# Optimization experiments

Measured on AMD Instinct MI355X. Metric: run time of the kernel, lower is better.

The kernel has to match this reference:

```python
import jax, jax.numpy as jnp
import numpy as np

C = 64  # in_dim

def _dwpw(x, w_dw, w_pw):
    # depthwise 1x1x1 conv (groups=C, no bias) == per-channel scale
    x = x * w_dw[None, :, None, None, None]
    # pointwise 1x1x1 conv (no bias) == channel mixing matmul
    return jnp.einsum('bcdhw,oc->bodhw', x, w_pw)

def setup_inputs() -> dict:
    key = jax.random.key(0)
    ks = jax.random.split(key, 8)
    B, D, H, W = 2, 16, 16, 16
    x = jax.random.normal(ks[0], (B, C, D, H, W), dtype=jnp.float32)
    s = 1.0 / np.sqrt(C)
    q_dw = jax.random.normal(ks[1], (C,), dtype=jnp.float32) * s
    q_pw = jax.random.normal(ks[2], (C, C), dtype=jnp.float32) * s
    k_dw = jax.random.normal(ks[3], (C,), dtype=jnp.float32) * s
    k_pw = jax.random.normal(ks[4], (C, C), dtype=jnp.float32) * s
    v_dw = jax.random.normal(ks[5], (C,), dtype=jnp.float32) * s
    v_pw = jax.random.normal(ks[6], (C, C), dtype=jnp.float32) * s
    gamma = jnp.zeros((1,), dtype=jnp.float32) + 0.1  # nonzero so output depends on attention
    return {"x": x, "q_dw": q_dw, "q_pw": q_pw, "k_dw": k_dw, "k_pw": k_pw,
            "v_dw": v_dw, "v_pw": v_pw, "gamma": gamma}

def reference(x, q_dw, q_pw, k_dw, k_pw, v_dw, v_pw, gamma):
    B, Cc, D, H, W = x.shape
    N = D * H * W
    q = _dwpw(x, q_dw, q_pw).reshape(B, Cc, N)  # [B,C,N]
    k = _dwpw(x, k_dw, k_pw).reshape(B, Cc, N)
    v = _dwpw(x, v_dw, v_pw).reshape(B, Cc, N)
    # energy[b,i,j] = sum_c q[b,c,i] * k[b,c,j]
    energy = jnp.einsum('bci,bcj->bij', q, k)
    attn = jax.nn.softmax(energy, axis=-1)  # softmax over j
    # out[b,c,i] = sum_j v[b,c,j] * attn[b,i,j]
    out = jnp.einsum('bcj,bij->bci', v, attn).reshape(B, Cc, D, H, W)
    return gamma * out + x
```

## Files before the change

kernel.cpp:

```cpp
#include <hip/hip_runtime.h>
#include <hip/hip_bf16.h>

#define NPOS 4096
#define CDIM 64
#define BATCH 2
#define JSPLIT 16
#define JCHUNK (NPOS / JSPLIT)
#define RPB 128
#define PSTR 72

typedef __attribute__((ext_vector_type(8))) short bf16x8;
typedef __attribute__((ext_vector_type(4))) short short4b;
typedef __attribute__((ext_vector_type(4))) float f32x4;
typedef __attribute__((ext_vector_type(4))) unsigned int u32x4;
typedef __attribute__((ext_vector_type(2))) unsigned int u32x2;

static __device__ __forceinline__ unsigned int fbits(float f) {
    union { float f; unsigned int u; } v; v.f = f; return v.u;
}
static __device__ __forceinline__ float bffloat(unsigned int hi16) {
    union { unsigned int u; float f; } v; v.u = hi16; return v.f;
}
static __device__ __forceinline__ unsigned int pk2bf(float a, float b) {
    return ((fbits(a) + 0x8000u) >> 16) | ((fbits(b) + 0x8000u) & 0xffff0000u);
}
static __device__ __forceinline__ short f2bs(float f) {
    return (short)(unsigned short)((fbits(f) + 0x8000u) >> 16);
}

__global__ __launch_bounds__(64) void qkv_kernel(
    const float* __restrict__ x,
    const float* __restrict__ q_dw, const float* __restrict__ q_pw,
    const float* __restrict__ k_dw, const float* __restrict__ k_pw,
    const float* __restrict__ v_dw, const float* __restrict__ v_pw,
    short* __restrict__ qT, short* __restrict__ kT, short* __restrict__ vM)
{
    const int bid  = blockIdx.x;
    const int p    = bid >> 9;
    const int np   = bid & 511;
    const int b    = np >> 8;
    const int n0   = (np & 255) << 4;
    const int lane = threadIdx.x;
    const int col  = lane & 15;
    const int quad = lane >> 4;
    const int n    = n0 + col;

    const float* pw = (p == 0) ? q_pw : (p == 1) ? k_pw : v_pw;
    const float* dw = (p == 0) ? q_dw : (p == 1) ? k_dw : v_dw;

    bf16x8 xf0, xf1;
    float dv0[8], dv1[8];
    #pragma unroll
    for (int j = 0; j < 8; ++j) {
        xf0[j] = f2bs(x[(size_t)(b * CDIM + quad * 8 + j) * NPOS + n]);
        xf1[j] = f2bs(x[(size_t)(b * CDIM + 32 + quad * 8 + j) * NPOS + n]);
        dv0[j] = dw[quad * 8 + j];
        dv1[j] = dw[32 + quad * 8 + j];
    }

    #pragma unroll
    for (int os = 0; os < 4; ++os) {
        const float* pr = pw + (os * 16 + col) * 64 + quad * 8;
        bf16x8 wf0, wf1;
        #pragma unroll
        for (int j = 0; j < 8; ++j) {
            wf0[j] = f2bs(pr[j] * dv0[j]);
            wf1[j] = f2bs(pr[32 + j] * dv1[j]);
        }
        f32x4 d = (f32x4){0.f, 0.f, 0.f, 0.f};
        if (p < 2) {
            d = __builtin_amdgcn_mfma_f32_16x16x32_bf16(wf0, xf0, d, 0, 0, 0);
            d = __builtin_amdgcn_mfma_f32_16x16x32_bf16(wf1, xf1, d, 0, 0, 0);
            short* dst = p ? kT : qT;
            *(u32x2*)(dst + (size_t)(b * NPOS + n) * CDIM + os * 16 + quad * 4) =
                (u32x2){pk2bf(d[0], d[1]), pk2bf(d[2], d[3])};
        } else {
            d = __builtin_amdgcn_mfma_f32_16x16x32_bf16(xf0, wf0, d, 0, 0, 0);
            d = __builtin_amdgcn_mfma_f32_16x16x32_bf16(xf1, wf1, d, 0, 0, 0);
            *(u32x2*)(vM + (size_t)(b * CDIM + os * 16 + col) * NPOS + n0 + quad * 4) =
                (u32x2){pk2bf(d[0], d[1]), pk2bf(d[2], d[3])};
        }
    }
}

__global__ __launch_bounds__(256, 3) void attn_kernel(
    const short* __restrict__ qT, const short* __restrict__ kT,
    const short* __restrict__ vM,
    unsigned short* __restrict__ Opart, float* __restrict__ lacc)
{
    const int gid  = blockIdx.x;
    const int jc   = gid & (JSPLIT - 1);
    const int rb   = (gid >> 4) & 31;
    const int b    = gid >> 9;
    const int t    = threadIdx.x;
    const int wave = t >> 6;
    const int lane = t & 63;
    const int col  = lane & 15;
    const int quad = lane >> 4;

    __shared__ __align__(16) short Pw[4][32 * PSTR];

    const short* qTb = qT + (size_t)b * NPOS * CDIM;
    const short* kTb = kT + (size_t)b * NPOS * CDIM;
    const short* vb  = vM + (size_t)b * CDIM * NPOS;

    const int i0 = rb * RPB + wave * 32;

    bf16x8 qf[2][2];
    #pragma unroll
    for (int rs = 0; rs < 2; ++rs) {
        const short* qp = qTb + (size_t)(i0 + rs * 16 + col) * CDIM + quad * 8;
        qf[rs][0] = *(const bf16x8*)qp;
        qf[rs][1] = *(const bf16x8*)(qp + 32);
    }

    f32x4 oacc[2][4];
    #pragma unroll
    for (int rs = 0; rs < 2; ++rs)
        #pragma unroll
        for (int cb = 0; cb < 4; ++cb) oacc[rs][cb] = (f32x4){0.f, 0.f, 0.f, 0.f};
    float lp[2] = {0.f, 0.f};

    short* Pme = Pw[wave];

    #pragma unroll
    for (int jt = 0; jt < JCHUNK / 64; ++jt) {
        const int j0 = jc * JCHUNK + jt * 64;

        bf16x8 kf[4][2], vf[4][2];
        #pragma unroll
        for (int ct = 0; ct < 4; ++ct) {
            const short* kp = kTb + (size_t)(j0 + ct * 16 + col) * CDIM + quad * 8;
            kf[ct][0] = *(const bf16x8*)kp;
            kf[ct][1] = *(const bf16x8*)(kp + 32);
        }
        #pragma unroll
        for (int cb = 0; cb < 4; ++cb) {
            const short* vp = vb + (size_t)(cb * 16 + col) * NPOS + j0 + quad * 8;
            vf[cb][0] = *(const bf16x8*)vp;
            vf[cb][1] = *(const bf16x8*)(vp + 32);
        }

        #pragma unroll
        for (int ct = 0; ct < 4; ++ct) {
            #pragma unroll
            for (int rs = 0; rs < 2; ++rs) {
                f32x4 a = (f32x4){0.f, 0.f, 0.f, 0.f};
                a = __builtin_amdgcn_mfma_f32_16x16x32_bf16(kf[ct][0], qf[rs][0], a, 0, 0, 0);
                a = __builtin_amdgcn_mfma_f32_16x16x32_bf16(kf[ct][1], qf[rs][1], a, 0, 0, 0);
                float p0 = __expf(a[0]), p1 = __expf(a[1]);
                float p2 = __expf(a[2]), p3 = __expf(a[3]);
                lp[rs] += (p0 + p1) + (p2 + p3);
                *(short4b*)(Pme + (rs * 16 + col) * PSTR + ct * 16 + quad * 4) =
                    (short4b){f2bs(p0), f2bs(p1), f2bs(p2), f2bs(p3)};
            }
        }

        bf16x8 pf[2][2];
        #pragma unroll
        for (int rs = 0; rs < 2; ++rs) {
            const short* pp = Pme + (rs * 16 + col) * PSTR + quad * 8;
            pf[rs][0] = *(const bf16x8*)pp;
            pf[rs][1] = *(const bf16x8*)(pp + 32);
        }

        #pragma unroll
        for (int cb = 0; cb < 4; ++cb)
            #pragma unroll
            for (int rs = 0; rs < 2; ++rs) {
                oacc[rs][cb] = __builtin_amdgcn_mfma_f32_16x16x32_bf16(vf[cb][0], pf[rs][0], oacc[rs][cb], 0, 0, 0);
                oacc[rs][cb] = __builtin_amdgcn_mfma_f32_16x16x32_bf16(vf[cb][1], pf[rs][1], oacc[rs][cb], 0, 0, 0);
            }
    }

    #pragma unroll
    for (int rs = 0; rs < 2; ++rs) {
        lp[rs] += __shfl_xor(lp[rs], 16, 64);
        lp[rs] += __shfl_xor(lp[rs], 32, 64);
    }
    if (quad == 0) {
        #pragma unroll
        for (int rs = 0; rs < 2; ++rs)
            lacc[(size_t)(jc * BATCH + b) * NPOS + i0 + rs * 16 + col] = lp[rs];
    }

    unsigned short* Ob = Opart + (size_t)(jc * BATCH + b) * CDIM * NPOS;
    #pragma unroll
    for (int rs = 0; rs < 2; ++rs)
        #pragma unroll
        for (int cb = 0; cb < 4; ++cb)
            #pragma unroll
            for (int r = 0; r < 4; ++r)
                Ob[(size_t)(cb * 16 + quad * 4 + r) * NPOS + i0 + rs * 16 + col] =
                    (unsigned short)f2bs(oacc[rs][cb][r]);
}

__global__ __launch_bounds__(256) void combine_kernel(
    const unsigned short* __restrict__ Opart, const float* __restrict__ lacc,
    const float* __restrict__ x, const float* __restrict__ gamma,
    float* __restrict__ out)
{
    int b  = blockIdx.x >> 7;
    int n0 = (blockIdx.x & 127) << 5;
    __shared__ float linv[32];
    int t = threadIdx.x;
    if (t < 32) {
        float s = 0.f;
        #pragma unroll
        for (int jc = 0; jc < JSPLIT; ++jc)
            s += lacc[(size_t)(jc * BATCH + b) * NPOS + n0 + t];
        linv[t] = gamma[0] / s;
    }
    __syncthreads();

    int c = t >> 2, ns = (t & 3) * 8;
    float acc[8];
    #pragma unroll
    for (int k = 0; k < 8; ++k) acc[k] = 0.f;
    #pragma unroll
    for (int jc = 0; jc < JSPLIT; ++jc) {
        const unsigned short* Ob = Opart + ((size_t)(jc * BATCH + b) * CDIM + c) * NPOS + n0 + ns;
        u32x4 w = *(const u32x4*)Ob;
        #pragma unroll
        for (int j = 0; j < 4; ++j) {
            acc[2 * j]     += bffloat(w[j] << 16);
            acc[2 * j + 1] += bffloat(w[j] & 0xffff0000u);
        }
    }
    const float* xb = x + ((size_t)b * CDIM + c) * NPOS + n0 + ns;
    float* ob = out + ((size_t)b * CDIM + c) * NPOS + n0 + ns;
    #pragma unroll
    for (int k = 0; k < 2; ++k) {
        f32x4 x4 = *(const f32x4*)(xb + k * 4);
        f32x4 r;
        #pragma unroll
        for (int j = 0; j < 4; ++j)
            r[j] = fmaf(acc[k * 4 + j], linv[ns + k * 4 + j], x4[j]);
        *(f32x4*)(ob + k * 4) = r;
    }
}

extern "C" void kernel_launch(void* const* d_in, const int* in_sizes, int n_in,
                              void* d_out, int out_size, void* d_ws, size_t ws_size,
                              hipStream_t stream) {
    const float* x     = (const float*)d_in[0];
    const float* q_dw  = (const float*)d_in[1];
    const float* q_pw  = (const float*)d_in[2];
    const float* k_dw  = (const float*)d_in[3];
    const float* k_pw  = (const float*)d_in[4];
    const float* v_dw  = (const float*)d_in[5];
    const float* v_pw  = (const float*)d_in[6];
    const float* gamma = (const float*)d_in[7];
    float* out = (float*)d_out;

    char* ws = (char*)d_ws;
    short* qT             = (short*)(ws);
    short* kT             = (short*)(ws + (1u << 20));
    short* vM             = (short*)(ws + (2u << 20));
    unsigned short* Opart = (unsigned short*)(ws + (3u << 20));
    float* lacc           = (float*)(ws + (3u << 20) +
                                     (size_t)JSPLIT * BATCH * CDIM * NPOS * 2);

    qkv_kernel<<<3 * BATCH * 256, 64, 0, stream>>>(
        x, q_dw, q_pw, k_dw, k_pw, v_dw, v_pw, qT, kT, vM);
    attn_kernel<<<BATCH * 32 * JSPLIT, 256, 0, stream>>>(qT, kT, vM, Opart, lacc);
    combine_kernel<<<BATCH * 128, 256, 0, stream>>>(Opart, lacc, x, gamma, out);
}
```

Before: 118.1 us.

## Stage K/V tiles in shared memory with register prefetch and halve J-split

The attention kernel now loads each 64-position K and V tile from global memory once per block, cooperatively across threads, into padded LDS buffers. All four waves read their MFMA operands from LDS instead of each wave fetching the same K/V data from global memory. The next tile is prefetched into registers while the current one is computed. JSPLIT drops from 16 to 8 and launch bounds drop to 2 blocks per CU, giving longer per-block loops and fewer partial outputs, at the cost of fewer blocks, less occupancy and two barriers per tile.

```diff
diff --git a/kernel.cpp b/kernel.cpp
--- a/kernel.cpp
+++ b/kernel.cpp
@@ -4,10 +4,12 @@
 #define NPOS 4096
 #define CDIM 64
 #define BATCH 2
-#define JSPLIT 16
+#define JSPLIT 8
 #define JCHUNK (NPOS / JSPLIT)
+#define NTILE (JCHUNK / 64)
 #define RPB 128
 #define PSTR 72
+#define KSTR 68
 
 typedef __attribute__((ext_vector_type(8))) short bf16x8;
 typedef __attribute__((ext_vector_type(4))) short short4b;
@@ -83,21 +85,23 @@
     }
 }
 
-__global__ __launch_bounds__(256, 3) void attn_kernel(
+__global__ __launch_bounds__(256, 2) void attn_kernel(
     const short* __restrict__ qT, const short* __restrict__ kT,
     const short* __restrict__ vM,
     unsigned short* __restrict__ Opart, float* __restrict__ lacc)
 {
     const int gid  = blockIdx.x;
     const int jc   = gid & (JSPLIT - 1);
-    const int rb   = (gid >> 4) & 31;
-    const int b    = gid >> 9;
+    const int rb   = (gid >> 3) & 31;
+    const int b    = gid >> 8;
     const int t    = threadIdx.x;
     const int wave = t >> 6;
     const int lane = t & 63;
     const int col  = lane & 15;
     const int quad = lane >> 4;
 
+    __shared__ __align__(16) short Ks[2][64 * KSTR];
+    __shared__ __align__(16) short Vs[2][64 * KSTR];
     __shared__ __align__(16) short Pw[4][32 * PSTR];
 
     const short* qTb = qT + (size_t)b * NPOS * CDIM;
@@ -105,6 +109,8 @@
     const short* vb  = vM + (size_t)b * CDIM * NPOS;
 
     const int i0 = rb * RPB + wave * 32;
+
+    const int r0 = t >> 3, r1 = (t + 256) >> 3, g8 = (t & 7) * 8;
 
     bf16x8 qf[2][2];
     #pragma unroll
@@ -122,21 +128,48 @@
     float lp[2] = {0.f, 0.f};
 
     short* Pme = Pw[wave];
-
-    #pragma unroll
-    for (int jt = 0; jt < JCHUNK / 64; ++jt) {
-        const int j0 = jc * JCHUNK + jt * 64;
+    const int jbase = jc * JCHUNK;
+
+    bf16x8 pk0, pk1, pv0, pv1;
+    {
+        const int j0 = jbase;
+        pk0 = *(const bf16x8*)(kTb + (size_t)(j0 + r0) * CDIM + g8);
+        pk1 = *(const bf16x8*)(kTb + (size_t)(j0 + r1) * CDIM + g8);
+        pv0 = *(const bf16x8*)(vb + (size_t)r0 * NPOS + j0 + g8);
+        pv1 = *(const bf16x8*)(vb + (size_t)r1 * NPOS + j0 + g8);
+    }
+
+    for (int jt = 0; jt < NTILE; ++jt) {
+        const int buf = jt & 1;
+        const int j0  = jbase + jt * 64;
+
+        __syncthreads();
+
+        *(bf16x8*)(Ks[buf] + r0 * KSTR + g8) = pk0;
+        *(bf16x8*)(Ks[buf] + r1 * KSTR + g8) = pk1;
+        *(bf16x8*)(Vs[buf] + r0 * KSTR + g8) = pv0;
+        *(bf16x8*)(Vs[buf] + r1 * KSTR + g8) = pv1;
+
+        {
+            const int jn = (jt + 1 < NTILE) ? jbase + (jt + 1) * 64 : jbase;
+            pk0 = *(const bf16x8*)(kTb + (size_t)(jn + r0) * CDIM + g8);
+            pk1 = *(const bf16x8*)(kTb + (size_t)(jn + r1) * CDIM + g8);
+            pv0 = *(const bf16x8*)(vb + (size_t)r0 * NPOS + jn + g8);
+            pv1 = *(const bf16x8*)(vb + (size_t)r1 * NPOS + jn + g8);
+        }
+
+        __syncthreads();
 
         bf16x8 kf[4][2], vf[4][2];
         #pragma unroll
         for (int ct = 0; ct < 4; ++ct) {
-            const short* kp = kTb + (size_t)(j0 + ct * 16 + col) * CDIM + quad * 8;
+            const short* kp = Ks[buf] + (ct * 16 + col) * KSTR + quad * 8;
             kf[ct][0] = *(const bf16x8*)kp;
             kf[ct][1] = *(const bf16x8*)(kp + 32);
         }
         #pragma unroll
         for (int cb = 0; cb < 4; ++cb) {
-            const short* vp = vb + (size_t)(cb * 16 + col) * NPOS + j0 + quad * 8;
+            const short* vp = Vs[buf] + (cb * 16 + col) * KSTR + quad * 8;
             vf[cb][0] = *(const bf16x8*)vp;
             vf[cb][1] = *(const bf16x8*)(vp + 32);
         }
```

Result: no change. 118.6 us (+0.5%).

## Fuse split-K combine into attention kernel via last-block atomic counter

Applied to the files above, without the earlier changes.

Removes the separate combine kernel launch. Each attention block bumps a per-row-block atomic counter after writing its partial output. The last of the JSPLIT blocks for that row block then reduces all partials and writes the final residual output. This saves a kernel launch and its tail, but adds a memset launch and threadfences, and the combine work is now serialized onto 64 blocks with larger per-thread accumulators.

```diff
diff --git a/kernel.cpp b/kernel.cpp
--- a/kernel.cpp
+++ b/kernel.cpp
@@ -86,7 +86,10 @@
 __global__ __launch_bounds__(256, 3) void attn_kernel(
     const short* __restrict__ qT, const short* __restrict__ kT,
     const short* __restrict__ vM,
-    unsigned short* __restrict__ Opart, float* __restrict__ lacc)
+    unsigned short* __restrict__ Opart, float* __restrict__ lacc,
+    int* __restrict__ cnt,
+    const float* __restrict__ x, const float* __restrict__ gamma,
+    float* __restrict__ out)
 {
     const int gid  = blockIdx.x;
     const int jc   = gid & (JSPLIT - 1);
@@ -193,50 +196,55 @@
             for (int r = 0; r < 4; ++r)
                 Ob[(size_t)(cb * 16 + quad * 4 + r) * NPOS + i0 + rs * 16 + col] =
                     (unsigned short)f2bs(oacc[rs][cb][r]);
-}
-
-__global__ __launch_bounds__(256) void combine_kernel(
-    const unsigned short* __restrict__ Opart, const float* __restrict__ lacc,
-    const float* __restrict__ x, const float* __restrict__ gamma,
-    float* __restrict__ out)
-{
-    int b  = blockIdx.x >> 7;
-    int n0 = (blockIdx.x & 127) << 5;
-    __shared__ float linv[32];
-    int t = threadIdx.x;
-    if (t < 32) {
+
+    __shared__ int is_last;
+    __threadfence();
+    if (t == 0) {
+        int old = atomicAdd(&cnt[b * 32 + rb], 1);
+        is_last = (old == JSPLIT - 1) ? 1 : 0;
+    }
+    __syncthreads();
+    if (!is_last) return;
+    __threadfence();
+
+    __shared__ float linv[RPB];
+    const int n0 = rb * RPB;
+    if (t < RPB) {
         float s = 0.f;
         #pragma unroll
-        for (int jc = 0; jc < JSPLIT; ++jc)
-            s += lacc[(size_t)(jc * BATCH + b) * NPOS + n0 + t];
+        for (int j = 0; j < JSPLIT; ++j)
+            s += lacc[(size_t)(j * BATCH + b) * NPOS + n0 + t];
         linv[t] = gamma[0] / s;
     }
     __syncthreads();
 
-    int c = t >> 2, ns = (t & 3) * 8;
-    float acc[8];
-    #pragma unroll
-    for (int k = 0; k < 8; ++k) acc[k] = 0.f;
-    #pragma unroll
-    for (int jc = 0; jc < JSPLIT; ++jc) {
-        const unsigned short* Ob = Opart + ((size_t)(jc * BATCH + b) * CDIM + c) * NPOS + n0 + ns;
-        u32x4 w = *(const u32x4*)Ob;
-        #pragma unroll
-        for (int j = 0; j < 4; ++j) {
-            acc[2 * j]     += bffloat(w[j] << 16);
-            acc[2 * j + 1] += bffloat(w[j] & 0xffff0000u);
-        }
-    }
-    const float* xb = x + ((size_t)b * CDIM + c) * NPOS + n0 + ns;
-    float* ob = out + ((size_t)b * CDIM + c) * NPOS + n0 + ns;
-    #pragma unroll
-    for (int k = 0; k < 2; ++k) {
-        f32x4 x4 = *(const f32x4*)(xb + k * 4);
+    const int c  = t >> 2;
+    const int nl = (t & 3) * 32;
+    float acc[32];
+    #pragma unroll
+    for (int k = 0; k < 32; ++k) acc[k] = 0.f;
+    for (int j = 0; j < JSPLIT; ++j) {
+        const unsigned short* Op = Opart +
+            ((size_t)(j * BATCH + b) * CDIM + c) * NPOS + n0 + nl;
+        #pragma unroll
+        for (int h = 0; h < 4; ++h) {
+            u32x4 w = *(const u32x4*)(Op + h * 8);
+            #pragma unroll
+            for (int d = 0; d < 4; ++d) {
+                acc[h * 8 + 2 * d]     += bffloat(w[d] << 16);
+                acc[h * 8 + 2 * d + 1] += bffloat(w[d] & 0xffff0000u);
+            }
+        }
+    }
+    const size_t base = ((size_t)b * CDIM + c) * NPOS + n0 + nl;
+    #pragma unroll
+    for (int k = 0; k < 8; ++k) {
+        f32x4 xv = *(const f32x4*)(x + base + k * 4);
         f32x4 r;
         #pragma unroll
-        for (int j = 0; j < 4; ++j)
-            r[j] = fmaf(acc[k * 4 + j], linv[ns + k * 4 + j], x4[j]);
-        *(f32x4*)(ob + k * 4) = r;
+        for (int d = 0; d < 4; ++d)
+            r[d] = fmaf(acc[k * 4 + d], linv[nl + k * 4 + d], xv[d]);
+        *(f32x4*)(out + base + k * 4) = r;
     }
 }
 
@@ -260,9 +268,11 @@
     unsigned short* Opart = (unsigned short*)(ws + (3u << 20));
     float* lacc           = (float*)(ws + (3u << 20) +
                                      (size_t)JSPLIT * BATCH * CDIM * NPOS * 2);
-
+    int* cnt              = (int*)((char*)lacc + (size_t)JSPLIT * BATCH * NPOS * 4);
+
+    hipMemsetAsync(cnt, 0, BATCH * 32 * sizeof(int), stream);
     qkv_kernel<<<3 * BATCH * 256, 64, 0, stream>>>(
         x, q_dw, q_pw, k_dw, k_pw, v_dw, v_pw, qT, kT, vM);
-    attn_kernel<<<BATCH * 32 * JSPLIT, 256, 0, stream>>>(qT, kT, vM, Opart, lacc);
-    combine_kernel<<<BATCH * 128, 256, 0, stream>>>(Opart, lacc, x, gamma, out);
-}
+    attn_kernel<<<BATCH * 32 * JSPLIT, 256, 0, stream>>>(
+        qT, kT, vM, Opart, lacc, cnt, x, gamma, out);
+}
```

Result: slower. 285.4 us (+141.8%).
